# Optimization experiments

Measured on AMD Instinct MI355X. Metric: run time of the kernel, lower is better.

Reference implementation:

```python
import jax, jax.numpy as jnp
import numpy as np

JITTER = 0.001

def se_kernel(X, X2, length_scale):
    # exp(-||x/ls - x2/ls||^2), scalar length scale
    X = X / length_scale
    X2 = X2 / length_scale
    d2 = (jnp.sum(X * X, axis=1)[:, None]
          - 2.0 * X @ X2.T
          + jnp.sum(X2 * X2, axis=1)[None, :])
    return jnp.exp(-d2)

def kron2(A, B):
    # torch kronecker(): einsum('ab,cd->acbd').view(a*c, b*d)
    return jnp.einsum('ab,cd->acbd', A, B).reshape(A.shape[0] * B.shape[0], A.shape[1] * B.shape[1])

def setup_inputs() -> dict:
    key = jax.random.key(0)
    k = jax.random.split(key, 6)
    Ns, Nt, Ms, Mt = 64, 100, 64, 100
    latlong = jax.random.normal(k[0], (Ns, 2), dtype=jnp.float32) * 5000.0
    elev = jax.random.normal(k[1], (Ns, 1), dtype=jnp.float32) * 50.0
    space = jnp.concatenate([latlong, elev], axis=1)
    time = jnp.linspace(0.0, 5.0, Nt, dtype=jnp.float32)[:, None]
    stData = jax.random.normal(k[2], (Ns, Nt), dtype=jnp.float32)
    t_latlong = jax.random.normal(k[3], (Ms, 2), dtype=jnp.float32) * 5000.0
    t_elev = jax.random.normal(k[4], (Ms, 1), dtype=jnp.float32) * 50.0
    test_space = jnp.concatenate([t_latlong, t_elev], axis=1)
    test_time = jnp.linspace(0.05, 5.05, Mt, dtype=jnp.float32)[:, None]
    return {
        'space_coordinates': space,
        'time_coordinates': time,
        'stData': stData,
        'test_space_coordinates': test_space,
        'test_time_coordinates': test_time,
        'log_latlong_length_scale': jnp.log(jnp.float32(4300.0)),
        'log_elevation_length_scale': jnp.log(jnp.float32(30.0)),
        'log_time_length_scale': jnp.log(jnp.float32(0.25)),
        'log_noise_variance': jnp.log(jnp.float32(0.1)),
        'log_signal_variance': jnp.log(jnp.float32(1.0)),
        'bias': jnp.zeros((Ns, 1), dtype=jnp.float32),
        'gain': jnp.ones((1,), dtype=jnp.float32),
    }

def reference(space_coordinates, time_coordinates, stData,
              test_space_coordinates, test_time_coordinates,
              log_latlong_length_scale, log_elevation_length_scale,
              log_time_length_scale, log_noise_variance, log_signal_variance,
              bias, gain):
    Ns = space_coordinates.shape[0]
    Nt = time_coordinates.shape[0]
    Ms = test_space_coordinates.shape[0]
    Mt = test_time_coordinates.shape[0]

    # ---- update(): build sigma_inverse and alpha on the training grid ----
    stData_cali = stData * gain + bias  # [Ns,Nt], bias broadcast over time
    ll = se_kernel(space_coordinates[:, 0:2], space_coordinates[:, 0:2], jnp.exp(log_latlong_length_scale))
    el = se_kernel(space_coordinates[:, 2:3], space_coordinates[:, 2:3], jnp.exp(log_elevation_length_scale))
    spatial_kernel = ll * el + jnp.eye(Ns, dtype=ll.dtype) * JITTER
    temporal_kernel = se_kernel(time_coordinates, time_coordinates, jnp.exp(log_time_length_scale)) + jnp.eye(Nt, dtype=ll.dtype) * JITTER
    wS, VS = jnp.linalg.eigh(spatial_kernel)
    wT, VT = jnp.linalg.eigh(temporal_kernel)
    V_st = kron2(VT, VS)                    # [Nt*Ns, Nt*Ns]
    ev_st = jnp.outer(wT, wS).reshape(-1)   # kron of eigenvalues, time-major
    inv_d = 1.0 / (ev_st + jnp.exp(log_noise_variance))
    sigma_inverse = (V_st * inv_d[None, :]) @ V_st.T
    alpha = sigma_inverse @ stData_cali.T.reshape(-1, 1)  # time-major vec

    # ---- forward() on test grid ----
    t_ll = se_kernel(test_space_coordinates[:, 0:2], space_coordinates[:, 0:2], jnp.exp(log_latlong_length_scale))
    t_el = se_kernel(test_space_coordinates[:, 2:3], space_coordinates[:, 2:3], jnp.exp(log_elevation_length_scale))
    test_spatial = t_ll * t_el                              # [Ms,Ns]
    test_temporal = se_kernel(test_time_coordinates, time_coordinates, jnp.exp(log_time_length_scale))  # [Mt,Nt]
    A = kron2(test_temporal, test_spatial)                  # [Mt*Ms, Nt*Ns]

    yPred = (A @ alpha).reshape(Mt, Ms).T                   # [Ms,Mt]
    # fused batched quadratic form replaces the per-row Python loop
    yVar = jnp.exp(log_signal_variance) - jnp.sum(A * (A @ sigma_inverse), axis=1)
    yVar = yVar.reshape(Mt, Ms).T                           # [Ms,Mt]
    return yPred, yVar
```

## Files before the change

### kernel.cpp

```cpp
#include <hip/hip_runtime.h>
#include <math.h>

#define JITTER 0.001f

enum {
  OFF_KS    = 0,
  OFF_KT    = 4096,
  OFF_Y     = 14096,
  OFF_EWS   = 20496,
  OFF_VS    = 20560,
  OFF_EWT   = 24656,
  OFF_VT    = 24756,
  OFF_P1    = 34756,
  OFF_TILDE = 41156,
  OFF_M1    = 47556,
  OFF_GS    = 53956,
  OFF_GT    = 58052,
  OFF_U2    = 68052,
  OFF_W2    = 78052,
  OFF_Z     = 82148,
  WS_FLOATS = 88548
};

#define BUILD2_TOTAL (4096 + 10000 + 6400)

__global__ void __launch_bounds__(256) build2_kernel(
    const float* __restrict__ space, const float* __restrict__ timec,
    const float* __restrict__ stData, const float* __restrict__ tspace,
    const float* __restrict__ ttime, const float* __restrict__ l_ll,
    const float* __restrict__ l_el, const float* __restrict__ l_t,
    const float* __restrict__ bias, const float* __restrict__ gain,
    float* __restrict__ ws)
{
  int idx = blockIdx.x * blockDim.x + threadIdx.x;
  if (idx >= BUILD2_TOTAL) return;
  float inv_ll = expf(-l_ll[0]);
  float inv_el = expf(-l_el[0]);
  float inv_t  = expf(-l_t[0]);
  if (idx < 4096) {
    int i = idx >> 6, j = idx & 63;
    float dx0 = (tspace[i*3+0] - space[j*3+0]) * inv_ll;
    float dx1 = (tspace[i*3+1] - space[j*3+1]) * inv_ll;
    float dz  = (tspace[i*3+2] - space[j*3+2]) * inv_el;
    ws[OFF_KS + idx] = expf(-(dx0*dx0 + dx1*dx1)) * expf(-(dz*dz));
  } else if (idx < 14096) {
    int k = idx - 4096;
    int j = k / 100, t = k % 100;
    float d = (ttime[j] - timec[t]) * inv_t;
    ws[OFF_KT + k] = expf(-d*d);
  } else {
    int k = idx - 14096;
    int s = k / 100;
    ws[OFF_Y + k] = stData[k] * gain[0] + bias[s];
  }
}

template<int N, int SWEEPS, int SPATIAL>
__device__ __forceinline__ void jacobi_body(
    const float* __restrict__ c0, const float* __restrict__ c1, float ia, float ib,
    float* __restrict__ wout, float* __restrict__ Vout, float* lds)
{
  constexpr int SA  = N + 1;
  constexpr int SW  = (N + 7) & ~3;
  constexpr int NP  = N / 2;
  constexpr int NTH = 1024;
  constexpr int NC  = SW / 4;
  constexpr int NB  = NP * (NP + 1) / 2;
  constexpr int NWI = NP * NC;
  float*  A   = lds;
  float*  W   = A + N * SA;
  float4* par = (float4*)(W + N * SW);
  const int tid = threadIdx.x;

  int k1a = -1, k2a = -1, k1b = -1, k2b = -1;
  {
    int b = tid;
    if (b < NB) {
      int k1 = 0, rem = b;
      while (rem >= NP - k1) { rem -= NP - k1; ++k1; }
      k1a = k1; k2a = k1 + rem;
    }
    b = tid + NTH;
    if (b < NB) {
      int k1 = 0, rem = b;
      while (rem >= NP - k1) { rem -= NP - k1; ++k1; }
      k1b = k1; k2b = k1 + rem;
    }
  }

  for (int idx = tid; idx < N * N; idx += NTH) {
    int i = idx / N, j = idx - i * N;
    float v;
    if (SPATIAL) {
      float dx0 = (c0[i*3+0] - c0[j*3+0]) * ia;
      float dx1 = (c0[i*3+1] - c0[j*3+1]) * ia;
      float dz  = (c0[i*3+2] - c0[j*3+2]) * ib;
      v = expf(-(dx0*dx0 + dx1*dx1)) * expf(-(dz*dz));
    } else {
      float d = (c1[i] - c1[j]) * ia;
      v = expf(-d*d);
    }
    if (i == j) v += JITTER;
    A[i * SA + j] = v;
    if (j < SW) W[i * SW + j] = (i == j) ? 1.0f : 0.0f;
  }
  __syncthreads();

  for (int sw = 0; sw < SWEEPS; ++sw) {
    for (int r = 0; r < N - 1; ++r) {
      if (tid < NP) {
        int p, q;
        if (tid == 0) { p = N - 1; q = r; }
        else {
          p = r + tid;  if (p >= N - 1) p -= N - 1;
          q = r - tid;  if (q < 0)      q += N - 1;
        }
        if (p > q) { int t = p; p = q; q = t; }
        float apq = A[p * SA + q];
        float app = A[p * SA + p];
        float aqq = A[q * SA + q];
        float c, s;
        if (fabsf(apq) < 1e-36f) { c = 1.0f; s = 0.0f; }
        else {
          float theta = (aqq - app) / (2.0f * apq);
          float tt = 1.0f / (fabsf(theta) + sqrtf(1.0f + theta * theta));
          if (theta < 0.0f) tt = -tt;
          c = 1.0f / sqrtf(1.0f + tt * tt);
          s = tt * c;
        }
        par[tid] = make_float4(c, s, __int_as_float(p), __int_as_float(q));
      }
      __syncthreads();

      if (k1a >= 0) {
        float4 P1 = par[k1a], P2 = par[k2a];
        float c1 = P1.x, s1 = P1.y;
        int p1 = __float_as_int(P1.z), q1 = __float_as_int(P1.w);
        float c2 = P2.x, s2 = P2.y;
        int p2 = __float_as_int(P2.z), q2 = __float_as_int(P2.w);
        float m00 = A[p1*SA+p2], m01 = A[p1*SA+q2];
        float m10 = A[q1*SA+p2], m11 = A[q1*SA+q2];
        float t00 = c1*m00 - s1*m10, t01 = c1*m01 - s1*m11;
        float t10 = s1*m00 + c1*m10, t11 = s1*m01 + c1*m11;
        float n00 = c2*t00 - s2*t01, n01 = s2*t00 + c2*t01;
        float n10 = c2*t10 - s2*t11, n11 = s2*t10 + c2*t11;
        A[p1*SA+p2] = n00; A[p1*SA+q2] = n01;
        A[q1*SA+p2] = n10; A[q1*SA+q2] = n11;
        if (k1a != k2a) {
          A[p2*SA+p1] = n00; A[p2*SA+q1] = n10;
          A[q2*SA+p1] = n01; A[q2*SA+q1] = n11;
        }
      }
      if (NB > NTH && k1b >= 0) {
        float4 P1 = par[k1b], P2 = par[k2b];
        float c1 = P1.x, s1 = P1.y;
        int p1 = __float_as_int(P1.z), q1 = __float_as_int(P1.w);
        float c2 = P2.x, s2 = P2.y;
        int p2 = __float_as_int(P2.z), q2 = __float_as_int(P2.w);
        float m00 = A[p1*SA+p2], m01 = A[p1*SA+q2];
        float m10 = A[q1*SA+p2], m11 = A[q1*SA+q2];
        float t00 = c1*m00 - s1*m10, t01 = c1*m01 - s1*m11;
        float t10 = s1*m00 + c1*m10, t11 = s1*m01 + c1*m11;
        float n00 = c2*t00 - s2*t01, n01 = s2*t00 + c2*t01;
        float n10 = c2*t10 - s2*t11, n11 = s2*t10 + c2*t11;
        A[p1*SA+p2] = n00; A[p1*SA+q2] = n01;
        A[q1*SA+p2] = n10; A[q1*SA+q2] = n11;
        if (k1b != k2b) {
          A[p2*SA+p1] = n00; A[p2*SA+q1] = n10;
          A[q2*SA+p1] = n01; A[q2*SA+q1] = n11;
        }
      }
      {
        int w = tid;
        if (w < NWI) {
          int k = w / NC, ch = w - k * NC;
          float4 P = par[k];
          int p = __float_as_int(P.z), q = __float_as_int(P.w);
          float4 wp = ((float4*)W)[p * NC + ch];
          float4 wq = ((float4*)W)[q * NC + ch];
          float4 r0, r1;
          r0.x = P.x*wp.x - P.y*wq.x;  r1.x = P.y*wp.x + P.x*wq.x;
          r0.y = P.x*wp.y - P.y*wq.y;  r1.y = P.y*wp.y + P.x*wq.y;
          r0.z = P.x*wp.z - P.y*wq.z;  r1.z = P.y*wp.z + P.x*wq.z;
          r0.w = P.x*wp.w - P.y*wq.w;  r1.w = P.y*wp.w + P.x*wq.w;
          ((float4*)W)[p * NC + ch] = r0;
          ((float4*)W)[q * NC + ch] = r1;
        }
      }
      if (NWI > NTH) {
        int w = tid + NTH;
        if (w < NWI) {
          int k = w / NC, ch = w - k * NC;
          float4 P = par[k];
          int p = __float_as_int(P.z), q = __float_as_int(P.w);
          float4 wp = ((float4*)W)[p * NC + ch];
          float4 wq = ((float4*)W)[q * NC + ch];
          float4 r0, r1;
          r0.x = P.x*wp.x - P.y*wq.x;  r1.x = P.y*wp.x + P.x*wq.x;
          r0.y = P.x*wp.y - P.y*wq.y;  r1.y = P.y*wp.y + P.x*wq.y;
          r0.z = P.x*wp.z - P.y*wq.z;  r1.z = P.y*wp.z + P.x*wq.z;
          r0.w = P.x*wp.w - P.y*wq.w;  r1.w = P.y*wp.w + P.x*wq.w;
          ((float4*)W)[p * NC + ch] = r0;
          ((float4*)W)[q * NC + ch] = r1;
        }
      }
      __syncthreads();
    }
  }

  for (int idx = tid; idx < N * N; idx += NTH) {
    int i = idx / N, j = idx - i * N;
    Vout[idx] = W[i * SW + j];
  }
  for (int i = tid; i < N; i += NTH) wout[i] = A[i * SA + i];
}

__global__ void __launch_bounds__(1024) jacobi_kernel(
    const float* __restrict__ space, const float* __restrict__ timec,
    const float* __restrict__ l_ll, const float* __restrict__ l_el,
    const float* __restrict__ l_t,
    float* __restrict__ wS, float* __restrict__ VSo,
    float* __restrict__ wT, float* __restrict__ VTo)
{
  extern __shared__ float lds[];
  if (blockIdx.x == 0)
    jacobi_body<64, 6, 1>(space, nullptr, expf(-l_ll[0]), expf(-l_el[0]), wS, VSo, lds);
  else
    jacobi_body<100, 6, 0>(nullptr, timec, expf(-l_t[0]), 0.0f, wT, VTo, lds);
}

__global__ void __launch_bounds__(256) gemm_k(
    const float* __restrict__ A, const float* __restrict__ B,
    float* __restrict__ C, float* __restrict__ C2,
    int M, int N, int K, int tA, int tB, int mode,
    const float* __restrict__ w1, const float* __restrict__ w2,
    const float* __restrict__ scal)
{
  int idx = blockIdx.x * blockDim.x + threadIdx.x;
  if (idx >= M * N) return;
  int m = idx / N, n = idx - m * N;
  float nv = (scal != nullptr) ? expf(scal[0]) : 0.0f;
  float acc = 0.0f;
  for (int k = 0; k < K; ++k) {
    float a;
    if (tA == 2)      a = 1.0f / (w1[m] * w2[k] + nv);
    else if (tA == 1) a = A[k * M + m];
    else              a = A[m * K + k];
    float b = tB ? B[n * K + k] : B[k * N + n];
    acc += a * b;
  }
  if (mode == 4) { C[idx] = acc; C2[idx] = acc * acc; return; }
  float out;
  if (mode == 1)      out = acc / (w1[m] * w2[n] + nv);
  else if (mode == 3) out = nv - acc;
  else                out = acc;
  C[idx] = out;
}

extern "C" void kernel_launch(void* const* d_in, const int* in_sizes, int n_in,
                              void* d_out, int out_size, void* d_ws, size_t ws_size,
                              hipStream_t stream) {
  const float* space  = (const float*)d_in[0];
  const float* timec  = (const float*)d_in[1];
  const float* stData = (const float*)d_in[2];
  const float* tspace = (const float*)d_in[3];
  const float* ttime  = (const float*)d_in[4];
  const float* l_ll   = (const float*)d_in[5];
  const float* l_el   = (const float*)d_in[6];
  const float* l_t    = (const float*)d_in[7];
  const float* l_nv   = (const float*)d_in[8];
  const float* l_sv   = (const float*)d_in[9];
  const float* bias   = (const float*)d_in[10];
  const float* gain   = (const float*)d_in[11];
  float* ws  = (float*)d_ws;
  float* out = (float*)d_out;

  const int JAC_LDS = (100*101 + 100*104 + 50*4) * 4;
  hipFuncSetAttribute((const void*)jacobi_kernel,
                      hipFuncAttributeMaxDynamicSharedMemorySize, JAC_LDS);

  build2_kernel<<<(BUILD2_TOTAL + 255) / 256, 256, 0, stream>>>(
      space, timec, stData, tspace, ttime, l_ll, l_el, l_t, bias, gain, ws);

  jacobi_kernel<<<2, 1024, JAC_LDS, stream>>>(
      space, timec, l_ll, l_el, l_t,
      ws + OFF_EWS, ws + OFF_VS, ws + OFF_EWT, ws + OFF_VT);

  auto grid = [](int mn) { return dim3((mn + 255) / 256); };
  float* NUL = nullptr;

  gemm_k<<<grid(4096), 256, 0, stream>>>(ws + OFF_KS, ws + OFF_VS,
      ws + OFF_GS, ws + OFF_W2, 64, 64, 64, 0, 1, 4, NUL, NUL, NUL);
  gemm_k<<<grid(10000), 256, 0, stream>>>(ws + OFF_KT, ws + OFF_VT,
      ws + OFF_GT, ws + OFF_U2, 100, 100, 100, 0, 1, 4, NUL, NUL, NUL);
  gemm_k<<<grid(6400), 256, 0, stream>>>(ws + OFF_VS, ws + OFF_Y,
      ws + OFF_P1, NUL, 64, 100, 64, 0, 0, 0, NUL, NUL, NUL);
  gemm_k<<<grid(6400), 256, 0, stream>>>(ws + OFF_P1, ws + OFF_VT,
      ws + OFF_TILDE, NUL, 64, 100, 100, 0, 1, 1, ws + OFF_EWS, ws + OFF_EWT, l_nv);
  gemm_k<<<grid(6400), 256, 0, stream>>>(NUL, ws + OFF_U2,
      ws + OFF_Z, NUL, 64, 100, 100, 2, 1, 0, ws + OFF_EWS, ws + OFF_EWT, l_nv);
  gemm_k<<<grid(6400), 256, 0, stream>>>(ws + OFF_GS, ws + OFF_TILDE,
      ws + OFF_M1, NUL, 64, 100, 64, 0, 0, 0, NUL, NUL, NUL);
  gemm_k<<<grid(6400), 256, 0, stream>>>(ws + OFF_M1, ws + OFF_GT,
      out, NUL, 64, 100, 100, 0, 1, 0, NUL, NUL, NUL);
  gemm_k<<<grid(6400), 256, 0, stream>>>(ws + OFF_W2, ws + OFF_Z,
      out + 6400, NUL, 64, 100, 64, 0, 0, 3, NUL, NUL, l_sv);
}
```

Baseline: 1.106 ms.

## Fuse all stages into one cooperative kernel and add Jacobi early exit

Replaces the build kernel, the two-block Jacobi kernel and eight small GEMM launches with one cooperative kernel that uses grid-wide syncs between stages. The Jacobi eigensolver now stores only rotation cosine and sine, recomputes the pivot indices, updates only the upper triangle, skips rotations when the off-diagonal is negligible, and stops early once a sweep makes no rotation. The sweep cap rises to 10. This removes launch overhead and idle sweeps, at the cost of grid-sync overhead and possible accuracy or iteration-count differences from the new convergence threshold.

```diff
diff --git a/kernel.cpp b/kernel.cpp
--- a/kernel.cpp
+++ b/kernel.cpp
@@ -1,5 +1,8 @@
 #include <hip/hip_runtime.h>
+#include <hip/hip_cooperative_groups.h>
 #include <math.h>
+
+namespace cg = cooperative_groups;
 
 #define JITTER 0.001f
 
@@ -22,37 +25,15 @@
   WS_FLOATS = 88548
 };
 
-#define BUILD2_TOTAL (4096 + 10000 + 6400)
-
-__global__ void __launch_bounds__(256) build2_kernel(
-    const float* __restrict__ space, const float* __restrict__ timec,
-    const float* __restrict__ stData, const float* __restrict__ tspace,
-    const float* __restrict__ ttime, const float* __restrict__ l_ll,
-    const float* __restrict__ l_el, const float* __restrict__ l_t,
-    const float* __restrict__ bias, const float* __restrict__ gain,
-    float* __restrict__ ws)
-{
-  int idx = blockIdx.x * blockDim.x + threadIdx.x;
-  if (idx >= BUILD2_TOTAL) return;
-  float inv_ll = expf(-l_ll[0]);
-  float inv_el = expf(-l_el[0]);
-  float inv_t  = expf(-l_t[0]);
-  if (idx < 4096) {
-    int i = idx >> 6, j = idx & 63;
-    float dx0 = (tspace[i*3+0] - space[j*3+0]) * inv_ll;
-    float dx1 = (tspace[i*3+1] - space[j*3+1]) * inv_ll;
-    float dz  = (tspace[i*3+2] - space[j*3+2]) * inv_el;
-    ws[OFF_KS + idx] = expf(-(dx0*dx0 + dx1*dx1)) * expf(-(dz*dz));
-  } else if (idx < 14096) {
-    int k = idx - 4096;
-    int j = k / 100, t = k % 100;
-    float d = (ttime[j] - timec[t]) * inv_t;
-    ws[OFF_KT + k] = expf(-d*d);
-  } else {
-    int k = idx - 14096;
-    int s = k / 100;
-    ws[OFF_Y + k] = stData[k] * gain[0] + bias[s];
-  }
+#define BUILD_TOTAL (4096 + 10000 + 6400)
+
+__device__ __forceinline__ void pq_of(int k, int r, int Nm1, int& p, int& q) {
+  if (k == 0) { p = Nm1; q = r; }
+  else {
+    p = r + k; if (p >= Nm1) p -= Nm1;
+    q = r - k; if (q < 0)    q += Nm1;
+  }
+  if (p > q) { int t = p; p = q; q = t; }
 }
 
 template<int N, int SWEEPS, int SPATIAL>
@@ -67,9 +48,11 @@
   constexpr int NC  = SW / 4;
   constexpr int NB  = NP * (NP + 1) / 2;
   constexpr int NWI = NP * NC;
+  constexpr int Nm1 = N - 1;
   float*  A   = lds;
   float*  W   = A + N * SA;
-  float4* par = (float4*)(W + N * SW);
+  float2* par = (float2*)(W + N * SW);
+  int*  cflag = (int*)(par + NP);
   const int tid = threadIdx.x;
 
   int k1a = -1, k2a = -1, k1b = -1, k2b = -1;
@@ -102,110 +85,78 @@
     }
     if (i == j) v += JITTER;
     A[i * SA + j] = v;
-    if (j < SW) W[i * SW + j] = (i == j) ? 1.0f : 0.0f;
-  }
+  }
+  for (int idx = tid; idx < N * SW; idx += NTH) {
+    int i = idx / SW, j = idx - i * SW;
+    W[idx] = (i == j) ? 1.0f : 0.0f;
+  }
+  if (tid == 0) *cflag = 0;
   __syncthreads();
 
   for (int sw = 0; sw < SWEEPS; ++sw) {
-    for (int r = 0; r < N - 1; ++r) {
+    for (int r = 0; r < Nm1; ++r) {
       if (tid < NP) {
         int p, q;
-        if (tid == 0) { p = N - 1; q = r; }
-        else {
-          p = r + tid;  if (p >= N - 1) p -= N - 1;
-          q = r - tid;  if (q < 0)      q += N - 1;
-        }
-        if (p > q) { int t = p; p = q; q = t; }
+        pq_of(tid, r, Nm1, p, q);
         float apq = A[p * SA + q];
         float app = A[p * SA + p];
         float aqq = A[q * SA + q];
-        float c, s;
-        if (fabsf(apq) < 1e-36f) { c = 1.0f; s = 0.0f; }
-        else {
+        float c = 1.0f, s = 0.0f;
+        if (fabsf(apq) > 1e-7f * (fabsf(app) + fabsf(aqq))) {
           float theta = (aqq - app) / (2.0f * apq);
           float tt = 1.0f / (fabsf(theta) + sqrtf(1.0f + theta * theta));
           if (theta < 0.0f) tt = -tt;
           c = 1.0f / sqrtf(1.0f + tt * tt);
           s = tt * c;
+          *cflag = 1;
         }
-        par[tid] = make_float4(c, s, __int_as_float(p), __int_as_float(q));
+        par[tid] = make_float2(c, s);
       }
       __syncthreads();
 
-      if (k1a >= 0) {
-        float4 P1 = par[k1a], P2 = par[k2a];
-        float c1 = P1.x, s1 = P1.y;
-        int p1 = __float_as_int(P1.z), q1 = __float_as_int(P1.w);
-        float c2 = P2.x, s2 = P2.y;
-        int p2 = __float_as_int(P2.z), q2 = __float_as_int(P2.w);
-        float m00 = A[p1*SA+p2], m01 = A[p1*SA+q2];
-        float m10 = A[q1*SA+p2], m11 = A[q1*SA+q2];
-        float t00 = c1*m00 - s1*m10, t01 = c1*m01 - s1*m11;
-        float t10 = s1*m00 + c1*m10, t11 = s1*m01 + c1*m11;
-        float n00 = c2*t00 - s2*t01, n01 = s2*t00 + c2*t01;
-        float n10 = c2*t10 - s2*t11, n11 = s2*t10 + c2*t11;
-        A[p1*SA+p2] = n00; A[p1*SA+q2] = n01;
-        A[q1*SA+p2] = n10; A[q1*SA+q2] = n11;
-        if (k1a != k2a) {
-          A[p2*SA+p1] = n00; A[p2*SA+q1] = n10;
-          A[q2*SA+p1] = n01; A[q2*SA+q1] = n11;
-        }
-      }
-      if (NB > NTH && k1b >= 0) {
-        float4 P1 = par[k1b], P2 = par[k2b];
-        float c1 = P1.x, s1 = P1.y;
-        int p1 = __float_as_int(P1.z), q1 = __float_as_int(P1.w);
-        float c2 = P2.x, s2 = P2.y;
-        int p2 = __float_as_int(P2.z), q2 = __float_as_int(P2.w);
-        float m00 = A[p1*SA+p2], m01 = A[p1*SA+q2];
-        float m10 = A[q1*SA+p2], m11 = A[q1*SA+q2];
-        float t00 = c1*m00 - s1*m10, t01 = c1*m01 - s1*m11;
-        float t10 = s1*m00 + c1*m10, t11 = s1*m01 + c1*m11;
-        float n00 = c2*t00 - s2*t01, n01 = s2*t00 + c2*t01;
-        float n10 = c2*t10 - s2*t11, n11 = s2*t10 + c2*t11;
-        A[p1*SA+p2] = n00; A[p1*SA+q2] = n01;
-        A[q1*SA+p2] = n10; A[q1*SA+q2] = n11;
-        if (k1b != k2b) {
-          A[p2*SA+p1] = n00; A[p2*SA+q1] = n10;
-          A[q2*SA+p1] = n01; A[q2*SA+q1] = n11;
-        }
-      }
-      {
-        int w = tid;
-        if (w < NWI) {
-          int k = w / NC, ch = w - k * NC;
-          float4 P = par[k];
-          int p = __float_as_int(P.z), q = __float_as_int(P.w);
-          float4 wp = ((float4*)W)[p * NC + ch];
-          float4 wq = ((float4*)W)[q * NC + ch];
-          float4 r0, r1;
-          r0.x = P.x*wp.x - P.y*wq.x;  r1.x = P.y*wp.x + P.x*wq.x;
-          r0.y = P.x*wp.y - P.y*wq.y;  r1.y = P.y*wp.y + P.x*wq.y;
-          r0.z = P.x*wp.z - P.y*wq.z;  r1.z = P.y*wp.z + P.x*wq.z;
-          r0.w = P.x*wp.w - P.y*wq.w;  r1.w = P.y*wp.w + P.x*wq.w;
-          ((float4*)W)[p * NC + ch] = r0;
-          ((float4*)W)[q * NC + ch] = r1;
-        }
-      }
-      if (NWI > NTH) {
-        int w = tid + NTH;
-        if (w < NWI) {
-          int k = w / NC, ch = w - k * NC;
-          float4 P = par[k];
-          int p = __float_as_int(P.z), q = __float_as_int(P.w);
-          float4 wp = ((float4*)W)[p * NC + ch];
-          float4 wq = ((float4*)W)[q * NC + ch];
-          float4 r0, r1;
-          r0.x = P.x*wp.x - P.y*wq.x;  r1.x = P.y*wp.x + P.x*wq.x;
-          r0.y = P.x*wp.y - P.y*wq.y;  r1.y = P.y*wp.y + P.x*wq.y;
-          r0.z = P.x*wp.z - P.y*wq.z;  r1.z = P.y*wp.z + P.x*wq.z;
-          r0.w = P.x*wp.w - P.y*wq.w;  r1.w = P.y*wp.w + P.x*wq.w;
-          ((float4*)W)[p * NC + ch] = r0;
-          ((float4*)W)[q * NC + ch] = r1;
-        }
-      }
+      auto do_block = [&](int k1, int k2) {
+        float2 P1 = par[k1], P2 = par[k2];
+        if (P1.y == 0.0f && P2.y == 0.0f) return;
+        int p1, q1, p2, q2;
+        pq_of(k1, r, Nm1, p1, q1);
+        pq_of(k2, r, Nm1, p2, q2);
+        int a00 = min(p1,p2)*SA + max(p1,p2);
+        int a01 = min(p1,q2)*SA + max(p1,q2);
+        int a10 = min(q1,p2)*SA + max(q1,p2);
+        int a11 = min(q1,q2)*SA + max(q1,q2);
+        float m00 = A[a00], m01 = A[a01], m10 = A[a10], m11 = A[a11];
+        float t00 = P1.x*m00 - P1.y*m10, t01 = P1.x*m01 - P1.y*m11;
+        float t10 = P1.y*m00 + P1.x*m10, t11 = P1.y*m01 + P1.x*m11;
+        A[a00] = P2.x*t00 - P2.y*t01;  A[a01] = P2.y*t00 + P2.x*t01;
+        A[a10] = P2.x*t10 - P2.y*t11;  A[a11] = P2.y*t10 + P2.x*t11;
+      };
+      if (k1a >= 0) do_block(k1a, k2a);
+      if (NB > NTH && k1b >= 0) do_block(k1b, k2b);
+
+      auto do_w = [&](int w) {
+        int k = w / NC, ch = w - k * NC;
+        float2 P = par[k];
+        if (P.y == 0.0f) return;
+        int p, q; pq_of(k, r, Nm1, p, q);
+        float4 wp = ((float4*)W)[p * NC + ch];
+        float4 wq = ((float4*)W)[q * NC + ch];
+        float4 r0, r1;
+        r0.x = P.x*wp.x - P.y*wq.x;  r1.x = P.y*wp.x + P.x*wq.x;
+        r0.y = P.x*wp.y - P.y*wq.y;  r1.y = P.y*wp.y + P.x*wq.y;
+        r0.z = P.x*wp.z - P.y*wq.z;  r1.z = P.y*wp.z + P.x*wq.z;
+        r0.w = P.x*wp.w - P.y*wq.w;  r1.w = P.y*wp.w + P.x*wq.w;
+        ((float4*)W)[p * NC + ch] = r0;
+        ((float4*)W)[q * NC + ch] = r1;
+      };
+      if (tid < NWI) do_w(tid);
+      if (NWI > NTH && tid + NTH < NWI) do_w(tid + NTH);
       __syncthreads();
     }
+    int done = (*cflag == 0);
+    __syncthreads();
+    if (tid == 0) *cflag = 0;
+    __syncthreads();
+    if (done) break;
   }
 
   for (int idx = tid; idx < N * N; idx += NTH) {
@@ -215,46 +166,130 @@
   for (int i = tid; i < N; i += NTH) wout[i] = A[i * SA + i];
 }
 
-__global__ void __launch_bounds__(1024) jacobi_kernel(
+__global__ void __launch_bounds__(1024) fused_kernel(
     const float* __restrict__ space, const float* __restrict__ timec,
+    const float* __restrict__ stData, const float* __restrict__ tspace,
+    const float* __restrict__ ttime,
     const float* __restrict__ l_ll, const float* __restrict__ l_el,
-    const float* __restrict__ l_t,
-    float* __restrict__ wS, float* __restrict__ VSo,
-    float* __restrict__ wT, float* __restrict__ VTo)
+    const float* __restrict__ l_t, const float* __restrict__ l_nv,
+    const float* __restrict__ l_sv,
+    const float* __restrict__ bias, const float* __restrict__ gain,
+    float* __restrict__ ws, float* __restrict__ out)
 {
   extern __shared__ float lds[];
-  if (blockIdx.x == 0)
-    jacobi_body<64, 6, 1>(space, nullptr, expf(-l_ll[0]), expf(-l_el[0]), wS, VSo, lds);
-  else
-    jacobi_body<100, 6, 0>(nullptr, timec, expf(-l_t[0]), 0.0f, wT, VTo, lds);
-}
-
-__global__ void __launch_bounds__(256) gemm_k(
-    const float* __restrict__ A, const float* __restrict__ B,
-    float* __restrict__ C, float* __restrict__ C2,
-    int M, int N, int K, int tA, int tB, int mode,
-    const float* __restrict__ w1, const float* __restrict__ w2,
-    const float* __restrict__ scal)
-{
-  int idx = blockIdx.x * blockDim.x + threadIdx.x;
-  if (idx >= M * N) return;
-  int m = idx / N, n = idx - m * N;
-  float nv = (scal != nullptr) ? expf(scal[0]) : 0.0f;
-  float acc = 0.0f;
-  for (int k = 0; k < K; ++k) {
-    float a;
-    if (tA == 2)      a = 1.0f / (w1[m] * w2[k] + nv);
-    else if (tA == 1) a = A[k * M + m];
-    else              a = A[m * K + k];
-    float b = tB ? B[n * K + k] : B[k * N + n];
-    acc += a * b;
-  }
-  if (mode == 4) { C[idx] = acc; C2[idx] = acc * acc; return; }
-  float out;
-  if (mode == 1)      out = acc / (w1[m] * w2[n] + nv);
-  else if (mode == 3) out = nv - acc;
-  else                out = acc;
-  C[idx] = out;
+  cg::grid_group grid = cg::this_grid();
+  const int bid = blockIdx.x, tid = threadIdx.x;
+
+  if (bid == 0) {
+    jacobi_body<64, 10, 1>(space, nullptr, expf(-l_ll[0]), expf(-l_el[0]),
+                           ws + OFF_EWS, ws + OFF_VS, lds);
+  } else if (bid == 1) {
+    jacobi_body<100, 10, 0>(nullptr, timec, expf(-l_t[0]), 0.0f,
+                            ws + OFF_EWT, ws + OFF_VT, lds);
+  } else {
+    int idx = (bid - 2) * 1024 + tid;
+    if (idx < BUILD_TOTAL) {
+      float inv_ll = expf(-l_ll[0]);
+      float inv_el = expf(-l_el[0]);
+      float inv_t  = expf(-l_t[0]);
+      if (idx < 4096) {
+        int i = idx >> 6, j = idx & 63;
+        float dx0 = (tspace[i*3+0] - space[j*3+0]) * inv_ll;
+        float dx1 = (tspace[i*3+1] - space[j*3+1]) * inv_ll;
+        float dz  = (tspace[i*3+2] - space[j*3+2]) * inv_el;
+        ws[OFF_KS + idx] = expf(-(dx0*dx0 + dx1*dx1)) * expf(-(dz*dz));
+      } else if (idx < 14096) {
+        int k = idx - 4096;
+        int j = k / 100, t = k % 100;
+        float d = (ttime[j] - timec[t]) * inv_t;
+        ws[OFF_KT + k] = expf(-d*d);
+      } else {
+        int k = idx - 14096;
+        int s = k / 100;
+        ws[OFF_Y + k] = stData[k] * gain[0] + bias[s];
+      }
+    }
+  }
+  grid.sync();
+
+  const int g = bid * 1024 + tid;
+
+  if (g < 4096) {
+    int i = g >> 6, j = g & 63;
+    float acc = 0.0f;
+    #pragma unroll 4
+    for (int k = 0; k < 64; ++k)
+      acc += ws[OFF_KS + i*64 + k] * ws[OFF_VS + j*64 + k];
+    ws[OFF_GS + g] = acc;
+    ws[OFF_W2 + g] = acc * acc;
+  } else if (g < 14096) {
+    int idx = g - 4096;
+    int i = idx / 100, j = idx - i * 100;
+    float acc = 0.0f;
+    #pragma unroll 4
+    for (int k = 0; k < 100; ++k)
+      acc += ws[OFF_KT + i*100 + k] * ws[OFF_VT + j*100 + k];
+    ws[OFF_GT + idx] = acc;
+    ws[OFF_U2 + idx] = acc * acc;
+  } else if (g < 20496) {
+    int idx = g - 14096;
+    int m = idx / 100, n = idx - m * 100;
+    float acc = 0.0f;
+    #pragma unroll 4
+    for (int k = 0; k < 64; ++k)
+      acc += ws[OFF_VS + m*64 + k] * ws[OFF_Y + k*100 + n];
+    ws[OFF_P1 + idx] = acc;
+  }
+  grid.sync();
+
+  {
+    float nv = expf(l_nv[0]);
+    if (g < 6400) {
+      int m = g / 100, n = g - m * 100;
+      float acc = 0.0f;
+      #pragma unroll 4
+      for (int k = 0; k < 100; ++k)
+        acc += ws[OFF_P1 + m*100 + k] * ws[OFF_VT + n*100 + k];
+      ws[OFF_TILDE + g] = acc / (ws[OFF_EWS + m] * ws[OFF_EWT + n] + nv);
+    } else if (g < 12800) {
+      int idx = g - 6400;
+      int m = idx / 100, n = idx - m * 100;
+      float wq = ws[OFF_EWS + m];
+      float acc = 0.0f;
+      #pragma unroll 4
+      for (int p = 0; p < 100; ++p)
+        acc += ws[OFF_U2 + n*100 + p] / (wq * ws[OFF_EWT + p] + nv);
+      ws[OFF_Z + idx] = acc;
+    }
+  }
+  grid.sync();
+
+  if (g < 6400) {
+    int m = g / 100, n = g - m * 100;
+    float acc = 0.0f;
+    #pragma unroll 4
+    for (int k = 0; k < 64; ++k)
+      acc += ws[OFF_GS + m*64 + k] * ws[OFF_TILDE + k*100 + n];
+    ws[OFF_M1 + g] = acc;
+  }
+  grid.sync();
+
+  if (g < 6400) {
+    int i = g / 100, j = g - i * 100;
+    float acc = 0.0f;
+    #pragma unroll 4
+    for (int k = 0; k < 100; ++k)
+      acc += ws[OFF_M1 + i*100 + k] * ws[OFF_GT + j*100 + k];
+    out[g] = acc;
+  } else if (g < 12800) {
+    int idx = g - 6400;
+    int i = idx / 100, j = idx - i * 100;
+    float acc = 0.0f;
+    #pragma unroll 4
+    for (int q = 0; q < 64; ++q)
+      acc += ws[OFF_W2 + i*64 + q] * ws[OFF_Z + q*100 + j];
+    out[6400 + idx] = expf(l_sv[0]) - acc;
+  }
 }
 
 extern "C" void kernel_launch(void* const* d_in, const int* in_sizes, int n_in,
@@ -275,34 +310,15 @@
   float* ws  = (float*)d_ws;
   float* out = (float*)d_out;
 
-  const int JAC_LDS = (100*101 + 100*104 + 50*4) * 4;
-  hipFuncSetAttribute((const void*)jacobi_kernel,
+  const int JAC_LDS = (100*101 + 100*104) * 4 + 50 * 8 + 32;
+  hipFuncSetAttribute((const void*)fused_kernel,
                       hipFuncAttributeMaxDynamicSharedMemorySize, JAC_LDS);
 
-  build2_kernel<<<(BUILD2_TOTAL + 255) / 256, 256, 0, stream>>>(
-      space, timec, stData, tspace, ttime, l_ll, l_el, l_t, bias, gain, ws);
-
-  jacobi_kernel<<<2, 1024, JAC_LDS, stream>>>(
-      space, timec, l_ll, l_el, l_t,
-      ws + OFF_EWS, ws + OFF_VS, ws + OFF_EWT, ws + OFF_VT);
-
-  auto grid = [](int mn) { return dim3((mn + 255) / 256); };
-  float* NUL = nullptr;
-
-  gemm_k<<<grid(4096), 256, 0, stream>>>(ws + OFF_KS, ws + OFF_VS,
-      ws + OFF_GS, ws + OFF_W2, 64, 64, 64, 0, 1, 4, NUL, NUL, NUL);
-  gemm_k<<<grid(10000), 256, 0, stream>>>(ws + OFF_KT, ws + OFF_VT,
-      ws + OFF_GT, ws + OFF_U2, 100, 100, 100, 0, 1, 4, NUL, NUL, NUL);
-  gemm_k<<<grid(6400), 256, 0, stream>>>(ws + OFF_VS, ws + OFF_Y,
-      ws + OFF_P1, NUL, 64, 100, 64, 0, 0, 0, NUL, NUL, NUL);
-  gemm_k<<<grid(6400), 256, 0, stream>>>(ws + OFF_P1, ws + OFF_VT,
-      ws + OFF_TILDE, NUL, 64, 100, 100, 0, 1, 1, ws + OFF_EWS, ws + OFF_EWT, l_nv);
-  gemm_k<<<grid(6400), 256, 0, stream>>>(NUL, ws + OFF_U2,
-      ws + OFF_Z, NUL, 64, 100, 100, 2, 1, 0, ws + OFF_EWS, ws + OFF_EWT, l_nv);
-  gemm_k<<<grid(6400), 256, 0, stream>>>(ws + OFF_GS, ws + OFF_TILDE,
-      ws + OFF_M1, NUL, 64, 100, 64, 0, 0, 0, NUL, NUL, NUL);
-  gemm_k<<<grid(6400), 256, 0, stream>>>(ws + OFF_M1, ws + OFF_GT,
-      out, NUL, 64, 100, 100, 0, 1, 0, NUL, NUL, NUL);
-  gemm_k<<<grid(6400), 256, 0, stream>>>(ws + OFF_W2, ws + OFF_Z,
-      out + 6400, NUL, 64, 100, 64, 0, 0, 3, NUL, NUL, l_sv);
+  void* args[] = {
+    (void*)&space, (void*)&timec, (void*)&stData, (void*)&tspace, (void*)&ttime,
+    (void*)&l_ll, (void*)&l_el, (void*)&l_t, (void*)&l_nv, (void*)&l_sv,
+    (void*)&bias, (void*)&gain, (void*)&ws, (void*)&out
+  };
+  hipLaunchCooperativeKernel((void*)fused_kernel, dim3(23), dim3(1024),
+                             args, JAC_LDS, stream);
 }
```

Measured after the change: 1.465 ms. 1.32x slower.
